# Kernel tuning notes

Measured on AMD Instinct MI355X. Metric: run time of the kernel, lower is better.

## Reference

```python
import jax, jax.numpy as jnp
import numpy as np
from jax import lax

KSIZE = 7
SIGMA = 5.0
ALPHA = 0.05


def _gaussian_kernel(ksize: int, sigma: float) -> jnp.ndarray:
    # 2D Gaussian, normalized to sum 1, replicated depthwise for 3 channels: (3,1,k,k)
    ax = jnp.arange(ksize, dtype=jnp.float32) - (ksize - 1) / 2.0
    g1 = jnp.exp(-(ax ** 2) / (2.0 * sigma ** 2))
    g2 = jnp.outer(g1, g1)
    g2 = g2 / jnp.sum(g2)
    return jnp.broadcast_to(g2[None, None], (3, 1, ksize, ksize)).astype(jnp.float32)


def _sobel_kernel() -> jnp.ndarray:
    # (2,1,3,3): channel 0 -> Ix, channel 1 -> Iy
    sx = jnp.array([[-1.0, 0.0, 1.0], [-2.0, 0.0, 2.0], [-1.0, 0.0, 1.0]], dtype=jnp.float32)
    sy = sx.T
    return jnp.stack([sx[None], sy[None]], axis=0)  # (2,1,3,3)


def setup_inputs() -> dict:
    key = jax.random.key(0)
    x = jax.random.normal(key, (1, 1, 4096, 4096), dtype=jnp.float32)
    return {"x": x, "sobel_k": _sobel_kernel(), "gauss_k": _gaussian_kernel(KSIZE, SIGMA)}


def _conv(x, k, pad, groups):
    return lax.conv_general_dilated(
        x, k, window_strides=(1, 1), padding=[(pad, pad), (pad, pad)],
        dimension_numbers=("NCHW", "OIHW", "NCHW"), feature_group_count=groups)


def reference(x, sobel_k, gauss_k):
    # ImageGradientsLayer: Sobel conv -> (1,2,H,W)
    g = _conv(x, sobel_k, 1, 1)
    Ix, Iy = g[:, 0:1], g[:, 1:2]
    # ChannelProductLayer -> (1,3,H,W)
    prod = jnp.concatenate([Ix * Ix, Iy * Iy, Ix * Iy], axis=1)
    # SecondMomentMatrixLayer: depthwise Gaussian blur, groups=3
    S = _conv(prod, gauss_k, KSIZE // 2, 3)
    Sxx, Syy, Sxy = S[0, 0], S[0, 1], S[0, 2]
    # CornerResponseLayer: R = det - alpha*trace^2
    tr = Sxx + Syy
    R = (Sxx * Syy - Sxy * Sxy - ALPHA * tr * tr)[None, None]  # (1,1,H,W)
    # NMSLayer: median threshold, 7x7 maxpool (stride 1, pad 3), keep maxima
    med = jnp.median(R)
    Rt = jnp.where(R >= med, R, jnp.float32(0.0))
    mp = lax.reduce_window(Rt, -jnp.inf, lax.max, (1, 1, 7, 7), (1, 1, 1, 1),
                           [(0, 0), (0, 0), (3, 3), (3, 3)])
    out = jnp.where(Rt != mp, jnp.float32(0.0), mp)
    return out
```

## Files before the change

kernel.cpp:

```cpp
#include <hip/hip_runtime.h>
#include <math.h>

#define N_IMG 4096
#define NBC   1024
#define H_OUT 32
#define HR    38
#define NPIX  (N_IMG * N_IMG)
#define HBLK  1024

struct W7 { float w[7]; };

__device__ __forceinline__ unsigned f2k(float f) {
    unsigned u = __float_as_uint(f);
    return (u & 0x80000000u) ? ~u : (u | 0x80000000u);
}
__device__ __forceinline__ float k2f(unsigned k) {
    unsigned u = (k & 0x80000000u) ? (k & 0x7fffffffu) : ~k;
    return __uint_as_float(u);
}

struct SelState { unsigned p1, p2, r1, r2; };

template<int BINS>
__device__ void locate_pair(const unsigned* h0, const unsigned* h1,
                            int shift, SelState& s)
{
    __shared__ unsigned scan[256];
    __shared__ unsigned resb[2], resr[2];
    const int tid = threadIdx.x;
    const int per = BINS / 256;
    const bool same = (h0 == h1);

    for (int q = 0; q < 2; q++) {
        if (q == 1 && same) break;
        const unsigned* h = q ? h1 : h0;
        const int base = tid * per;
        unsigned sum = 0;
        #pragma unroll
        for (int i = 0; i < per; i++) sum += h[base + i];
        __syncthreads();
        scan[tid] = sum;
        __syncthreads();
        unsigned v = sum;
        #pragma unroll
        for (int off = 1; off < 256; off <<= 1) {
            unsigned t = (tid >= off) ? scan[tid - off] : 0u;
            __syncthreads();
            v += t;
            scan[tid] = v;
            __syncthreads();
        }
        const unsigned excl = v - sum;
        #pragma unroll
        for (int w = 0; w < 2; w++) {
            const unsigned rank = w ? s.r2 : s.r1;
            const bool mine = w ? (same || q == 1) : (q == 0);
            if (mine && rank >= excl && rank < v) {
                unsigned rr = rank - excl;
                for (int i = 0; i < per; i++) {
                    unsigned c = h[base + i];
                    if (rr < c) { resb[w] = (unsigned)(base + i); resr[w] = rr; break; }
                    rr -= c;
                }
            }
        }
        __syncthreads();
    }
    s.p1 |= resb[0] << shift; s.r1 = resr[0];
    s.p2 |= resb[1] << shift; s.r2 = resr[1];
}

__device__ __forceinline__ SelState derive0(const unsigned* g0) {
    SelState s; s.p1 = 0u; s.p2 = 0u;
    s.r1 = (unsigned)(NPIX / 2 - 1); s.r2 = (unsigned)(NPIX / 2);
    locate_pair<4096>(g0, g0, 20, s);
    return s;
}
__device__ __forceinline__ void derive1(const unsigned* g1, SelState& s) {
    const unsigned* h1 = (s.p1 != s.p2) ? (g1 + 4096) : g1;
    locate_pair<4096>(g1, h1, 8, s);
}
__device__ __forceinline__ void derive2(const unsigned* g2, SelState& s) {
    const unsigned* h1 = (s.p1 != s.p2) ? (g2 + 256) : g2;
    locate_pair<256>(g2, h1, 0, s);
}

__global__ __launch_bounds__(256, 2) void harris_kernel(const float* __restrict__ x,
                                                        float* __restrict__ R,
                                                        unsigned* __restrict__ g0,
                                                        W7 wp)
{
    __shared__ unsigned histo[4096];
    const int tid = threadIdx.x;
    for (int i = tid; i < 4096; i += 256) histo[i] = 0;
    __syncthreads();

    const int row0 = blockIdx.y * H_OUT;
    const int jc   = blockIdx.x * NBC + tid * 4;
    const float* w = wp.w;
    const bool edge = (jc < 4) || (jc >= N_IMG - 8);

    float xm[12], xc[12], xp[12];
    float axx[7][4], ayy[7][4], axy[7][4];

    #pragma unroll
    for (int m = 0; m < 7; m++)
        #pragma unroll
        for (int o = 0; o < 4; o++) { axx[m][o] = 0.f; ayy[m][o] = 0.f; axy[m][o] = 0.f; }

    auto loadrow = [&](int ri, float* d) {
        if ((unsigned)ri < N_IMG) {
            const float* p = x + (size_t)ri * N_IMG;
            float4 v0 = make_float4(0.f,0.f,0.f,0.f), v2 = make_float4(0.f,0.f,0.f,0.f);
            if (jc >= 4) v0 = *(const float4*)(p + jc - 4);
            float4 v1 = *(const float4*)(p + jc);
            if (jc + 4 < N_IMG) v2 = *(const float4*)(p + jc + 4);
            d[0]=v0.x; d[1]=v0.y; d[2]=v0.z; d[3]=v0.w;
            d[4]=v1.x; d[5]=v1.y; d[6]=v1.z; d[7]=v1.w;
            d[8]=v2.x; d[9]=v2.y; d[10]=v2.z; d[11]=v2.w;
        } else {
            #pragma unroll
            for (int t = 0; t < 12; t++) d[t] = 0.f;
        }
    };

    loadrow(row0 - 4, xm);
    loadrow(row0 - 3, xc);

    int curb = -1; unsigned cnt = 0;

    auto step = [&](int r, int k, int dmin, bool emit) {
        const int ri = row0 + r - 3;
        loadrow(ri + 1, xp);

        if ((unsigned)ri < N_IMG) {
            float dc[12], rd[12];
            #pragma unroll
            for (int t = 0; t < 12; t++) {
                dc[t] = xm[t] + 2.f * xc[t] + xp[t];
                rd[t] = xp[t] - xm[t];
            }
            float ixv[10], iyv[10];
            #pragma unroll
            for (int t = 0; t < 10; t++) {
                ixv[t] = dc[t+2] - dc[t];
                iyv[t] = rd[t] + 2.f * rd[t+1] + rd[t+2];
            }
            if (edge) {
                #pragma unroll
                for (int t = 0; t < 10; t++)
                    if ((unsigned)(jc - 3 + t) >= N_IMG) { ixv[t] = 0.f; iyv[t] = 0.f; }
            }
            float sxx[4] = {0,0,0,0}, syy[4] = {0,0,0,0}, sxy[4] = {0,0,0,0};
            #pragma unroll
            for (int t = 0; t < 10; t++) {
                float ix = ixv[t], iy = iyv[t];
                float xx = ix*ix, yy = iy*iy, xy = ix*iy;
                #pragma unroll
                for (int o = 0; o < 4; o++) {
                    const int v = t - o;
                    if (v >= 0 && v < 7) {
                        sxx[o] = fmaf(w[v], xx, sxx[o]);
                        syy[o] = fmaf(w[v], yy, syy[o]);
                        sxy[o] = fmaf(w[v], xy, sxy[o]);
                    }
                }
            }
            #pragma unroll
            for (int d = 0; d < 7; d++) {
                if (d >= dmin) {
                    const int m = (k + d) % 7;
                    #pragma unroll
                    for (int o = 0; o < 4; o++) {
                        axx[m][o] = fmaf(w[6-d], sxx[o], axx[m][o]);
                        ayy[m][o] = fmaf(w[6-d], syy[o], ayy[m][o]);
                        axy[m][o] = fmaf(w[6-d], sxy[o], axy[m][o]);
                    }
                }
            }
        }

        if (emit) {
            float4 h;
            float* hp = &h.x;
            #pragma unroll
            for (int o = 0; o < 4; o++) {
                float ax = axx[k][o], ay = ayy[k][o], az = axy[k][o];
                axx[k][o] = 0.f; ayy[k][o] = 0.f; axy[k][o] = 0.f;
                float tr = ax + ay;
                hp[o] = ax*ay - az*az - 0.05f*tr*tr;
            }
            const int orow = row0 + r - 6;
            *(float4*)(R + (size_t)orow * N_IMG + jc) = h;
            #pragma unroll
            for (int o = 0; o < 4; o++) {
                int b = (int)(f2k(hp[o]) >> 20);
                if (b == curb) cnt++;
                else { if (curb >= 0) atomicAdd(&histo[curb], cnt); curb = b; cnt = 1; }
            }
        }
        #pragma unroll
        for (int t = 0; t < 12; t++) { xm[t] = xc[t]; xc[t] = xp[t]; }
    };

    #pragma unroll
    for (int rr = 0; rr < 7; ++rr)
        step(rr, rr, 6 - rr, rr == 6);
    for (int it = 1; it < 6; ++it) {
        #pragma unroll
        for (int k = 0; k < 7; ++k) {
            const int r = it * 7 + k;
            if (r < HR) step(r, k, 0, true);
        }
    }

    if (curb >= 0) atomicAdd(&histo[curb], cnt);
    __syncthreads();
    for (int i = tid; i < 4096; i += 256) {
        unsigned c = histo[i];
        if (c) atomicAdd(&g0[i], c);
    }
}

__global__ __launch_bounds__(256) void hist1_kernel(const float* __restrict__ R,
                                                    const unsigned* __restrict__ g0,
                                                    unsigned* __restrict__ g1)
{
    __shared__ unsigned h[2][4096];
    const int tid = threadIdx.x;
    for (int i = tid; i < 8192; i += 256) ((unsigned*)h)[i] = 0u;

    SelState s = derive0(g0);
    const unsigned p1 = s.p1, p2 = s.p2;
    const bool dual = (p1 != p2);
    const unsigned mask = 0xFFF00000u;
    const int shift = 8;

    const int n4 = NPIX / 4;
    const int stride = gridDim.x * 256;
    int curb1 = -1; unsigned cnt1 = 0;
    int curb2 = -1; unsigned cnt2 = 0;
    const float4* R4 = (const float4*)R;

    auto proc = [&](unsigned k) {
        if ((k & mask) == p1) {
            int b = (int)((k >> shift) & 4095u);
            if (b == curb1) cnt1++;
            else { if (cnt1) atomicAdd(&h[0][curb1], cnt1); curb1 = b; cnt1 = 1; }
        }
        if (dual && (k & mask) == p2) {
            int b = (int)((k >> shift) & 4095u);
            if (b == curb2) cnt2++;
            else { if (cnt2) atomicAdd(&h[1][curb2], cnt2); curb2 = b; cnt2 = 1; }
        }
    };

    int i = blockIdx.x * 256 + tid;
    for (; i + 3 * stride < n4; i += 4 * stride) {
        float4 va = R4[i];
        float4 vb = R4[i + stride];
        float4 vc = R4[i + 2 * stride];
        float4 vd = R4[i + 3 * stride];
        float vv[16] = {va.x, va.y, va.z, va.w, vb.x, vb.y, vb.z, vb.w,
                        vc.x, vc.y, vc.z, vc.w, vd.x, vd.y, vd.z, vd.w};
        #pragma unroll
        for (int t = 0; t < 16; t++) proc(f2k(vv[t]));
    }
    for (; i < n4; i += stride) {
        float4 va = R4[i];
        float vv[4] = {va.x, va.y, va.z, va.w};
        #pragma unroll
        for (int t = 0; t < 4; t++) proc(f2k(vv[t]));
    }
    if (cnt1) atomicAdd(&h[0][curb1], cnt1);
    if (cnt2) atomicAdd(&h[1][curb2], cnt2);
    __syncthreads();
    for (int j = tid; j < 4096; j += 256) {
        unsigned c0 = h[0][j]; if (c0) atomicAdd(&g1[j], c0);
        if (dual) { unsigned c1 = h[1][j]; if (c1) atomicAdd(&g1[4096 + j], c1); }
    }
}

__global__ __launch_bounds__(256) void hist2_kernel(const float* __restrict__ R,
                                                    const unsigned* __restrict__ g0,
                                                    const unsigned* __restrict__ g1,
                                                    unsigned* __restrict__ g2)
{
    __shared__ unsigned h[2][256];
    const int tid = threadIdx.x;
    for (int i = tid; i < 512; i += 256) ((unsigned*)h)[i] = 0u;

    SelState s = derive0(g0);
    derive1(g1, s);
    const unsigned p1 = s.p1, p2 = s.p2;
    const bool dual = (p1 != p2);
    const unsigned mask = 0xFFFFFF00u;

    const int n4 = NPIX / 4;
    const int stride = gridDim.x * 256;
    int curb1 = -1; unsigned cnt1 = 0;
    int curb2 = -1; unsigned cnt2 = 0;
    const float4* R4 = (const float4*)R;

    auto proc = [&](unsigned k) {
        if ((k & mask) == p1) {
            int b = (int)(k & 255u);
            if (b == curb1) cnt1++;
            else { if (cnt1) atomicAdd(&h[0][curb1], cnt1); curb1 = b; cnt1 = 1; }
        }
        if (dual && (k & mask) == p2) {
            int b = (int)(k & 255u);
            if (b == curb2) cnt2++;
            else { if (cnt2) atomicAdd(&h[1][curb2], cnt2); curb2 = b; cnt2 = 1; }
        }
    };

    int i = blockIdx.x * 256 + tid;
    for (; i + 3 * stride < n4; i += 4 * stride) {
        float4 va = R4[i];
        float4 vb = R4[i + stride];
        float4 vc = R4[i + 2 * stride];
        float4 vd = R4[i + 3 * stride];
        float vv[16] = {va.x, va.y, va.z, va.w, vb.x, vb.y, vb.z, vb.w,
                        vc.x, vc.y, vc.z, vc.w, vd.x, vd.y, vd.z, vd.w};
        #pragma unroll
        for (int t = 0; t < 16; t++) proc(f2k(vv[t]));
    }
    for (; i < n4; i += stride) {
        float4 va = R4[i];
        float vv[4] = {va.x, va.y, va.z, va.w};
        #pragma unroll
        for (int t = 0; t < 4; t++) proc(f2k(vv[t]));
    }
    if (cnt1) atomicAdd(&h[0][curb1], cnt1);
    if (cnt2) atomicAdd(&h[1][curb2], cnt2);
    __syncthreads();
    if (tid < 256) {
        unsigned c0 = h[0][tid]; if (c0) atomicAdd(&g2[tid], c0);
        if (dual) { unsigned c1 = h[1][tid]; if (c1) atomicAdd(&g2[256 + tid], c1); }
    }
}

__global__ __launch_bounds__(256) void init_kernel(unsigned* __restrict__ g)
{
    const int tid = threadIdx.x;
    for (int i = tid; i < 12800; i += 256) g[i] = 0u;
}

__global__ __launch_bounds__(256, 2) void nms_kernel(const float* __restrict__ R,
                                                     const unsigned* __restrict__ g0,
                                                     const unsigned* __restrict__ g1,
                                                     const unsigned* __restrict__ g2,
                                                     float* __restrict__ out)
{
    const int tid  = threadIdx.x;

    SelState s = derive0(g0);
    derive1(g1, s);
    derive2(g2, s);
    const float med = 0.5f * (k2f(s.p1) + k2f(s.p2));

    const int row0 = blockIdx.y * H_OUT;
    const int jc   = blockIdx.x * NBC + tid * 4;

    float vm[7][4];
    float ct[7][4];
    #pragma unroll
    for (int m = 0; m < 7; m++)
        #pragma unroll
        for (int o = 0; o < 4; o++) vm[m][o] = -INFINITY;

    auto loadrowT = [&](int ri, float* d) {
        if ((unsigned)ri < N_IMG) {
            const float* p = R + (size_t)ri * N_IMG;
            float4 v1 = *(const float4*)(p + jc);
            d[4] = (v1.x >= med) ? v1.x : 0.f;
            d[5] = (v1.y >= med) ? v1.y : 0.f;
            d[6] = (v1.z >= med) ? v1.z : 0.f;
            d[7] = (v1.w >= med) ? v1.w : 0.f;
            if (jc >= 4) {
                float4 v0 = *(const float4*)(p + jc - 4);
                d[0] = (v0.x >= med) ? v0.x : 0.f;
                d[1] = (v0.y >= med) ? v0.y : 0.f;
                d[2] = (v0.z >= med) ? v0.z : 0.f;
                d[3] = (v0.w >= med) ? v0.w : 0.f;
            } else { d[0]=d[1]=d[2]=d[3] = -INFINITY; }
            if (jc + 4 < N_IMG) {
                float4 v2 = *(const float4*)(p + jc + 4);
                d[8]  = (v2.x >= med) ? v2.x : 0.f;
                d[9]  = (v2.y >= med) ? v2.y : 0.f;
                d[10] = (v2.z >= med) ? v2.z : 0.f;
                d[11] = (v2.w >= med) ? v2.w : 0.f;
            } else { d[8]=d[9]=d[10]=d[11] = -INFINITY; }
        } else {
            #pragma unroll
            for (int t = 0; t < 12; t++) d[t] = -INFINITY;
        }
    };

    auto stepn = [&](int r, int k, int dmin, bool emit) {
        const int ri = row0 + r - 3;
        float a[12];
        loadrowT(ri, a);
        float hm[4];
        #pragma unroll
        for (int o = 0; o < 4; o++) {
            float m01 = fmaxf(a[o+1], a[o+2]);
            float m23 = fmaxf(a[o+3], a[o+4]);
            float m45 = fmaxf(a[o+5], a[o+6]);
            hm[o] = fmaxf(fmaxf(m01, m23), fmaxf(m45, a[o+7]));
            ct[k][o] = a[4+o];
        }
        #pragma unroll
        for (int d = 0; d < 7; d++) {
            if (d >= dmin) {
                const int m = (k + d) % 7;
                #pragma unroll
                for (int o = 0; o < 4; o++)
                    vm[m][o] = fmaxf(vm[m][o], hm[o]);
            }
        }
        if (emit) {
            float4 ov;
            float* op = &ov.x;
            #pragma unroll
            for (int o = 0; o < 4; o++) {
                float m = vm[k][o];
                vm[k][o] = -INFINITY;
                float c = ct[(k+4) % 7][o];
                op[o] = (c != m) ? 0.f : m;
            }
            const int orow = row0 + r - 6;
            *(float4*)(out + (size_t)orow * N_IMG + jc) = ov;
        }
    };

    #pragma unroll
    for (int rr = 0; rr < 7; ++rr)
        stepn(rr, rr, 6 - rr, rr == 6);
    for (int it = 1; it < 6; ++it) {
        #pragma unroll
        for (int k = 0; k < 7; ++k) {
            const int r = it * 7 + k;
            if (r < HR) stepn(r, k, 0, true);
        }
    }
}

extern "C" void kernel_launch(void* const* d_in, const int* in_sizes, int n_in,
                              void* d_out, int out_size, void* d_ws, size_t ws_size,
                              hipStream_t stream)
{
    const float* x = (const float*)d_in[0];
    float* R = (float*)d_ws;
    unsigned* g0 = (unsigned*)((char*)d_ws + (size_t)NPIX * 4);
    unsigned* g1 = g0 + 4096;
    unsigned* g2 = g1 + 8192;
    float* out = (float*)d_out;

    W7 wp;
    {
        double g[7], sm = 0.0;
        for (int i = 0; i < 7; i++) { double ax = (double)i - 3.0; g[i] = exp(-(ax*ax)/50.0); sm += g[i]; }
        for (int i = 0; i < 7; i++) wp.w[i] = (float)(g[i] / sm);
    }

    dim3 sgrid(N_IMG / NBC, N_IMG / H_OUT);

    init_kernel<<<1, 256, 0, stream>>>(g0);
    harris_kernel<<<sgrid, 256, 0, stream>>>(x, R, g0, wp);
    hist1_kernel<<<HBLK, 256, 0, stream>>>(R, g0, g1);
    hist2_kernel<<<HBLK, 256, 0, stream>>>(R, g0, g1, g2);
    nms_kernel<<<sgrid, 256, 0, stream>>>(R, g0, g1, g2, out);
}
```

Measured before the change: 274.2 us.

## Replicate global histograms to cut atomic contention and shrink NMS tile height

```diff
diff --git a/kernel.cpp b/kernel.cpp
--- a/kernel.cpp
+++ b/kernel.cpp
@@ -5,8 +5,11 @@
 #define NBC   1024
 #define H_OUT 32
 #define HR    38
+#define NMS_HOUT 16
+#define NMS_HR   22
 #define NPIX  (N_IMG * N_IMG)
 #define HBLK  1024
+#define NREP  8
 
 struct W7 { float w[7]; };
 
@@ -23,21 +26,27 @@
 
 template<int BINS>
 __device__ void locate_pair(const unsigned* h0, const unsigned* h1,
-                            int shift, SelState& s)
+                            int repstride, int shift, SelState& s)
 {
     __shared__ unsigned scan[256];
     __shared__ unsigned resb[2], resr[2];
     const int tid = threadIdx.x;
-    const int per = BINS / 256;
+    constexpr int per = BINS / 256;
     const bool same = (h0 == h1);
 
     for (int q = 0; q < 2; q++) {
         if (q == 1 && same) break;
         const unsigned* h = q ? h1 : h0;
         const int base = tid * per;
+        unsigned loc[per];
         unsigned sum = 0;
         #pragma unroll
-        for (int i = 0; i < per; i++) sum += h[base + i];
+        for (int i = 0; i < per; i++) {
+            unsigned c = 0;
+            #pragma unroll
+            for (int r = 0; r < NREP; r++) c += h[r * repstride + base + i];
+            loc[i] = c; sum += c;
+        }
         __syncthreads();
         scan[tid] = sum;
         __syncthreads();
@@ -57,8 +66,9 @@
             const bool mine = w ? (same || q == 1) : (q == 0);
             if (mine && rank >= excl && rank < v) {
                 unsigned rr = rank - excl;
+                #pragma unroll
                 for (int i = 0; i < per; i++) {
-                    unsigned c = h[base + i];
+                    unsigned c = loc[i];
                     if (rr < c) { resb[w] = (unsigned)(base + i); resr[w] = rr; break; }
                     rr -= c;
                 }
@@ -70,19 +80,19 @@
     s.p2 |= resb[1] << shift; s.r2 = resr[1];
 }
 
-__device__ __forceinline__ SelState derive0(const unsigned* g0) {
+__device__ __forceinline__ SelState derive0(const unsigned* g0r) {
     SelState s; s.p1 = 0u; s.p2 = 0u;
     s.r1 = (unsigned)(NPIX / 2 - 1); s.r2 = (unsigned)(NPIX / 2);
-    locate_pair<4096>(g0, g0, 20, s);
+    locate_pair<4096>(g0r, g0r, 4096, 20, s);
     return s;
 }
-__device__ __forceinline__ void derive1(const unsigned* g1, SelState& s) {
-    const unsigned* h1 = (s.p1 != s.p2) ? (g1 + 4096) : g1;
-    locate_pair<4096>(g1, h1, 8, s);
-}
-__device__ __forceinline__ void derive2(const unsigned* g2, SelState& s) {
-    const unsigned* h1 = (s.p1 != s.p2) ? (g2 + 256) : g2;
-    locate_pair<256>(g2, h1, 0, s);
+__device__ __forceinline__ void derive1(const unsigned* g1r, SelState& s) {
+    const unsigned* h1 = (s.p1 != s.p2) ? (g1r + 4096) : g1r;
+    locate_pair<4096>(g1r, h1, 8192, 8, s);
+}
+__device__ __forceinline__ void derive2(const unsigned* g2r, SelState& s) {
+    const unsigned* h1 = (s.p1 != s.p2) ? (g2r + 256) : g2r;
+    locate_pair<256>(g2r, h1, 512, 0, s);
 }
 
 __global__ __launch_bounds__(256, 2) void harris_kernel(const float* __restrict__ x,
@@ -216,9 +226,10 @@
 
     if (curb >= 0) atomicAdd(&histo[curb], cnt);
     __syncthreads();
+    unsigned* gdst = g0 + ((blockIdx.x + blockIdx.y) & (NREP - 1)) * 4096;
     for (int i = tid; i < 4096; i += 256) {
         unsigned c = histo[i];
-        if (c) atomicAdd(&g0[i], c);
+        if (c) atomicAdd(&gdst[i], c);
     }
 }
 
@@ -275,9 +286,10 @@
     if (cnt1) atomicAdd(&h[0][curb1], cnt1);
     if (cnt2) atomicAdd(&h[1][curb2], cnt2);
     __syncthreads();
+    unsigned* gdst = g1 + (blockIdx.x & (NREP - 1)) * 8192;
     for (int j = tid; j < 4096; j += 256) {
-        unsigned c0 = h[0][j]; if (c0) atomicAdd(&g1[j], c0);
-        if (dual) { unsigned c1 = h[1][j]; if (c1) atomicAdd(&g1[4096 + j], c1); }
+        unsigned c0 = h[0][j]; if (c0) atomicAdd(&gdst[j], c0);
+        if (dual) { unsigned c1 = h[1][j]; if (c1) atomicAdd(&gdst[4096 + j], c1); }
     }
 }
 
@@ -335,19 +347,21 @@
     if (cnt1) atomicAdd(&h[0][curb1], cnt1);
     if (cnt2) atomicAdd(&h[1][curb2], cnt2);
     __syncthreads();
+    unsigned* gdst = g2 + (blockIdx.x & (NREP - 1)) * 512;
     if (tid < 256) {
-        unsigned c0 = h[0][tid]; if (c0) atomicAdd(&g2[tid], c0);
-        if (dual) { unsigned c1 = h[1][tid]; if (c1) atomicAdd(&g2[256 + tid], c1); }
+        unsigned c0 = h[0][tid]; if (c0) atomicAdd(&gdst[tid], c0);
+        if (dual) { unsigned c1 = h[1][tid]; if (c1) atomicAdd(&gdst[256 + tid], c1); }
     }
 }
 
 __global__ __launch_bounds__(256) void init_kernel(unsigned* __restrict__ g)
 {
-    const int tid = threadIdx.x;
-    for (int i = tid; i < 12800; i += 256) g[i] = 0u;
-}
-
-__global__ __launch_bounds__(256, 2) void nms_kernel(const float* __restrict__ R,
+    const unsigned n = NREP * (4096u + 8192u + 512u);
+    for (unsigned i = blockIdx.x * 256u + threadIdx.x; i < n; i += gridDim.x * 256u)
+        g[i] = 0u;
+}
+
+__global__ __launch_bounds__(256, 4) void nms_kernel(const float* __restrict__ R,
                                                      const unsigned* __restrict__ g0,
                                                      const unsigned* __restrict__ g1,
                                                      const unsigned* __restrict__ g2,
@@ -360,7 +374,7 @@
     derive2(g2, s);
     const float med = 0.5f * (k2f(s.p1) + k2f(s.p2));
 
-    const int row0 = blockIdx.y * H_OUT;
+    const int row0 = blockIdx.y * NMS_HOUT;
     const int jc   = blockIdx.x * NBC + tid * 4;
 
     float vm[7][4];
@@ -438,11 +452,11 @@
     #pragma unroll
     for (int rr = 0; rr < 7; ++rr)
         stepn(rr, rr, 6 - rr, rr == 6);
-    for (int it = 1; it < 6; ++it) {
+    for (int it = 1; it < 4; ++it) {
         #pragma unroll
         for (int k = 0; k < 7; ++k) {
             const int r = it * 7 + k;
-            if (r < HR) stepn(r, k, 0, true);
+            if (r < NMS_HR) stepn(r, k, 0, true);
         }
     }
 }
@@ -454,8 +468,8 @@
     const float* x = (const float*)d_in[0];
     float* R = (float*)d_ws;
     unsigned* g0 = (unsigned*)((char*)d_ws + (size_t)NPIX * 4);
-    unsigned* g1 = g0 + 4096;
-    unsigned* g2 = g1 + 8192;
+    unsigned* g1 = g0 + NREP * 4096;
+    unsigned* g2 = g1 + NREP * 8192;
     float* out = (float*)d_out;
 
     W7 wp;
@@ -466,10 +480,11 @@
     }
 
     dim3 sgrid(N_IMG / NBC, N_IMG / H_OUT);
-
-    init_kernel<<<1, 256, 0, stream>>>(g0);
+    dim3 ngrid(N_IMG / NBC, N_IMG / NMS_HOUT);
+
+    init_kernel<<<64, 256, 0, stream>>>(g0);
     harris_kernel<<<sgrid, 256, 0, stream>>>(x, R, g0, wp);
     hist1_kernel<<<HBLK, 256, 0, stream>>>(R, g0, g1);
     hist2_kernel<<<HBLK, 256, 0, stream>>>(R, g0, g1, g2);
-    nms_kernel<<<sgrid, 256, 0, stream>>>(R, g0, g1, g2, out);
-}
+    nms_kernel<<<ngrid, 256, 0, stream>>>(R, g0, g1, g2, out);
+}
```

After: 316.5 us. +15.4%, slower.
